# Optimization experiments

Measured on AMD Instinct MI355X. Metric: run time of the kernel, lower is better.

## Reference

```python
import jax, jax.numpy as jnp
import numpy as np

B, T, D_MODEL, D_HIDDEN, MAX_SEQLEN = 4, 2048, 1024, 256, 2048


def setup_inputs() -> dict:
    key = jax.random.key(0)
    ks = jax.random.split(key, 8)
    s_in = 1.0 / np.sqrt(D_MODEL)
    s_out = 1.0 / np.sqrt(D_HIDDEN)
    # xavier_uniform bound for W_bias (fan_in = fan_out = MAX_SEQLEN)
    xb = np.sqrt(6.0 / (MAX_SEQLEN + MAX_SEQLEN))
    return {
        "q": jax.random.normal(ks[0], (B, T, D_MODEL), jnp.float32),
        "k": jax.random.normal(ks[1], (B, T, D_MODEL), jnp.float32),
        "v": jax.random.normal(ks[2], (B, T, D_MODEL), jnp.float32),
        "Wq": jax.random.normal(ks[3], (D_MODEL, D_HIDDEN), jnp.float32) * s_in,
        "Wk": jax.random.normal(ks[4], (D_MODEL, D_HIDDEN), jnp.float32) * s_in,
        "Wv": jax.random.normal(ks[5], (D_MODEL, D_HIDDEN), jnp.float32) * s_in,
        "Wo": jax.random.normal(ks[6], (D_HIDDEN, D_MODEL), jnp.float32) * s_out,
        "W_bias": jax.random.uniform(ks[7], (MAX_SEQLEN, MAX_SEQLEN), jnp.float32, -xb, xb),
    }


def reference(q, k, v, Wq, Wk, Wv, Wo, W_bias):
    Ti, Tj = q.shape[1], k.shape[1]
    Q = q @ Wq                      # [B,Ti,dh]
    K = k @ Wk                      # [B,Tj,dh]
    V = v @ Wv                      # [B,Tj,dh]
    pos_bias = W_bias[:Ti, :Tj][None]               # [1,Ti,Tj]
    # NOTE: source subtracts max over dim 0 (batch). For pos_bias that dim is 1,
    # so exp_pos_bias == exp(0) == ones -- reproduced faithfully here.
    max_key = jnp.max(K, axis=0, keepdims=True)      # [1,Tj,dh]
    max_pos_bias = jnp.max(pos_bias, axis=0, keepdims=True)
    exp_key = jnp.exp(K - max_key)                   # [B,Tj,dh]
    exp_pos_bias = jnp.exp(pos_bias - max_pos_bias)  # [1,Ti,Tj]
    num = jnp.einsum('ij,bjd->bid', exp_pos_bias[0], exp_key * V)  # [B,Ti,dh]
    den = jnp.einsum('ij,bjd->bid', exp_pos_bias[0], exp_key)      # [B,Ti,dh]
    Yt = jax.nn.sigmoid(Q) * num / den
    return Yt @ Wo                  # [B,Ti,d_model]
```

## Files before the change

kernel.cpp:

```cpp
#include <hip/hip_runtime.h>
#include <hip/hip_bf16.h>
#include <math.h>

#define B_   4
#define T_   2048
#define DM   1024
#define DH   256
#define M_   (B_*T_)

typedef __bf16 bf16;
typedef __attribute__((ext_vector_type(8))) __bf16 bf16x8;
typedef __attribute__((ext_vector_type(4))) float  f32x4;

__device__ inline float sigmoidf_(float x) { return 1.0f / (1.0f + __expf(-x)); }

__device__ inline int swz8(int r, int c) { return (((c >> 3) ^ (r & 7)) << 3); }

__global__ void transpose_cvt_all(const float* __restrict__ Wq, const float* __restrict__ Wk,
                                  const float* __restrict__ Wv, const float* __restrict__ Wo,
                                  bf16* __restrict__ Wq_t, bf16* __restrict__ Wk_t,
                                  bf16* __restrict__ Wv_t, bf16* __restrict__ Wo_t,
                                  float* __restrict__ nd)
{
    const int bid = blockIdx.x;
    if (bid >= 1024) {
        nd[(bid - 1024) * 256 + threadIdx.x] = 0.f;
        return;
    }
    __shared__ float tile[32][33];
    const int w = bid >> 8, t = bid & 255;
    const float* in; bf16* out; int R, C, sh;
    if      (w == 0) { in = Wq; out = Wq_t; R = DM; C = DH; sh = 3; }
    else if (w == 1) { in = Wk; out = Wk_t; R = DM; C = DH; sh = 3; }
    else if (w == 2) { in = Wv; out = Wv_t; R = DM; C = DH; sh = 3; }
    else             { in = Wo; out = Wo_t; R = DH; C = DM; sh = 5; }
    const int r0 = (t >> sh) * 32, c0 = (t & ((1 << sh) - 1)) * 32;
    const int tx = threadIdx.x & 31, ty = threadIdx.x >> 5;
    #pragma unroll
    for (int i = ty; i < 32; i += 8)
        tile[i][tx] = in[(long)(r0 + i) * C + c0 + tx];
    __syncthreads();
    #pragma unroll
    for (int i = ty; i < 32; i += 8)
        out[(long)(c0 + i) * R + r0 + tx] = (bf16)tile[tx][i];
}

__global__ __launch_bounds__(512, 6)
void gemm_proj(const float* __restrict__ qin, const float* __restrict__ kin,
               const float* __restrict__ vin,
               const bf16* __restrict__ Wq_t, const bf16* __restrict__ Wk_t,
               const bf16* __restrict__ Wv_t,
               bf16* __restrict__ Yb, bf16* __restrict__ Kb, bf16* __restrict__ Vb)
{
    __shared__ __align__(16) bf16 As[2][64][64];
    __shared__ __align__(16) bf16 Bs[2][128][64];

    const int z = blockIdx.z;
    const float* A  = (z == 0) ? qin  : (z == 1) ? kin  : vin;
    const bf16*  Wt = (z == 0) ? Wq_t : (z == 1) ? Wk_t : Wv_t;
    bf16*        C  = (z == 0) ? Yb   : (z == 1) ? Kb   : Vb;

    const int bid  = blockIdx.x;
    const int tile = (bid & 7) * 32 + (bid >> 3);
    const int m0 = (tile >> 1) * 64;
    const int n0 = (tile & 1) * 128;

    const int tid = threadIdx.x, lane = tid & 63, wave = tid >> 6;
    const int wr = wave >> 2, wc = wave & 3;
    const int q4 = lane >> 4, l16 = lane & 15;

    f32x4 acc[2][2] = {};
    const int ar = tid >> 3, ac8 = (tid & 7) * 8;
    const int br = tid >> 2, bc16 = (tid & 3) * 16;

    const float* aBase = &A[(long)(m0 + ar) * DM + ac8];
    const bf16*  bBase = &Wt[(long)(n0 + br) * DM + bc16];

    f32x4  pa0[2], pa1[2];
    bf16x8 pb0[2], pb1[2];
    #pragma unroll
    for (int p = 0; p < 2; ++p) {
        const float* ap = aBase + p * 64;
        pa0[p] = *(const f32x4*)ap; pa1[p] = *(const f32x4*)(ap + 4);
        const bf16* bp = bBase + p * 64;
        pb0[p] = *(const bf16x8*)bp; pb1[p] = *(const bf16x8*)(bp + 8);
    }
    {
        bf16x8 o;
        #pragma unroll
        for (int e = 0; e < 4; ++e) { o[e] = (bf16)pa0[0][e]; o[4 + e] = (bf16)pa1[0][e]; }
        *(bf16x8*)&As[0][ar][swz8(ar, ac8)]      = o;
        *(bf16x8*)&Bs[0][br][swz8(br, bc16)]     = pb0[0];
        *(bf16x8*)&Bs[0][br][swz8(br, bc16 + 8)] = pb1[0];
    }
    __syncthreads();

    #pragma unroll
    for (int s = 0; s < 16; ++s) {
        const int cs = s & 1;
        const int ns = cs ^ 1;
        if (s + 2 < 16) {
            const float* ap = aBase + (s + 2) * 64;
            pa0[cs] = *(const f32x4*)ap; pa1[cs] = *(const f32x4*)(ap + 4);
            const bf16* bp = bBase + (s + 2) * 64;
            pb0[cs] = *(const bf16x8*)bp; pb1[cs] = *(const bf16x8*)(bp + 8);
        }
        if (s + 1 < 16) {
            bf16x8 o;
            #pragma unroll
            for (int e = 0; e < 4; ++e) { o[e] = (bf16)pa0[ns][e]; o[4 + e] = (bf16)pa1[ns][e]; }
            *(bf16x8*)&As[ns][ar][swz8(ar, ac8)]      = o;
            *(bf16x8*)&Bs[ns][br][swz8(br, bc16)]     = pb0[ns];
            *(bf16x8*)&Bs[ns][br][swz8(br, bc16 + 8)] = pb1[ns];
        }
        #pragma unroll
        for (int kk = 0; kk < 64; kk += 32) {
            const int ra = wr * 32 + l16, rb = wc * 32 + l16;
            bf16x8 a0 = *(const bf16x8*)&As[cs][ra     ][swz8(ra,      kk + q4 * 8)];
            bf16x8 a1 = *(const bf16x8*)&As[cs][ra + 16][swz8(ra + 16, kk + q4 * 8)];
            bf16x8 b0 = *(const bf16x8*)&Bs[cs][rb     ][swz8(rb,      kk + q4 * 8)];
            bf16x8 b1 = *(const bf16x8*)&Bs[cs][rb + 16][swz8(rb + 16, kk + q4 * 8)];
            acc[0][0] = __builtin_amdgcn_mfma_f32_16x16x32_bf16(a0, b0, acc[0][0], 0, 0, 0);
            acc[0][1] = __builtin_amdgcn_mfma_f32_16x16x32_bf16(a0, b1, acc[0][1], 0, 0, 0);
            acc[1][0] = __builtin_amdgcn_mfma_f32_16x16x32_bf16(a1, b0, acc[1][0], 0, 0, 0);
            acc[1][1] = __builtin_amdgcn_mfma_f32_16x16x32_bf16(a1, b1, acc[1][1], 0, 0, 0);
        }
        __syncthreads();
    }
    #pragma unroll
    for (int i = 0; i < 2; ++i)
        #pragma unroll
        for (int j = 0; j < 2; ++j)
            #pragma unroll
            for (int r = 0; r < 4; ++r) {
                int gm = m0 + wr * 32 + i * 16 + q4 * 4 + r;
                int gn = n0 + wc * 32 + j * 16 + l16;
                float v = acc[i][j][r];
                C[(long)gm * DH + gn] = (bf16)((z == 0) ? sigmoidf_(v) : v);
            }
}

__global__ void reduce_kv(const bf16* __restrict__ Kb, const bf16* __restrict__ Vb,
                          float* __restrict__ numb, float* __restrict__ denb)
{
    __shared__ float red[2][4][B_][DH];
    const int tid = threadIdx.x;
    const int g = tid & 31, jj = tid >> 5;
    const int d8 = g * 8;
    const int j = blockIdx.x * 8 + jj;

    bf16x8 kx[B_], vx[B_];
    #pragma unroll
    for (int b = 0; b < B_; ++b) {
        kx[b] = *(const bf16x8*)&Kb[((long)b * T_ + j) * DH + d8];
        vx[b] = *(const bf16x8*)&Vb[((long)b * T_ + j) * DH + d8];
    }
    float sn[B_][8], sd[B_][8];
    #pragma unroll
    for (int e = 0; e < 8; ++e) {
        float k0 = (float)kx[0][e], k1 = (float)kx[1][e];
        float k2 = (float)kx[2][e], k3 = (float)kx[3][e];
        float mx = fmaxf(fmaxf(k0, k1), fmaxf(k2, k3));
        float e0 = __expf(k0 - mx), e1 = __expf(k1 - mx);
        float e2 = __expf(k2 - mx), e3 = __expf(k3 - mx);
        sn[0][e] = e0 * (float)vx[0][e]; sd[0][e] = e0;
        sn[1][e] = e1 * (float)vx[1][e]; sd[1][e] = e1;
        sn[2][e] = e2 * (float)vx[2][e]; sd[2][e] = e2;
        sn[3][e] = e3 * (float)vx[3][e]; sd[3][e] = e3;
    }
    #pragma unroll
    for (int b = 0; b < B_; ++b)
        #pragma unroll
        for (int e = 0; e < 8; ++e) {
            sn[b][e] += __shfl_xor(sn[b][e], 32);
            sd[b][e] += __shfl_xor(sd[b][e], 32);
        }
    const int w = tid >> 6;
    if ((tid & 32) == 0) {
        #pragma unroll
        for (int b = 0; b < B_; ++b)
            #pragma unroll
            for (int e = 0; e < 8; ++e) {
                red[0][w][b][d8 + e] = sn[b][e];
                red[1][w][b][d8 + e] = sd[b][e];
            }
    }
    __syncthreads();
    #pragma unroll
    for (int o = tid; o < 2 * B_ * DH; o += 256) {
        const int arr = o >> 10, b = (o >> 8) & 3, d = o & 255;
        float s = red[arr][0][b][d] + red[arr][1][b][d]
                + red[arr][2][b][d] + red[arr][3][b][d];
        float* dst = (o < 1024) ? &numb[o] : &denb[o - 1024];
        atomicAdd(dst, s);
    }
}

__global__ __launch_bounds__(512, 6)
void gemm_out(const bf16* __restrict__ Yb, const bf16* __restrict__ Wo_t,
              const float* __restrict__ numb, const float* __restrict__ denb,
              float* __restrict__ out)
{
    __shared__ __align__(16) bf16 As[2][64][64];
    __shared__ __align__(16) bf16 Bs[2][128][64];
    __shared__ float rv_s[DH];

    const int bid  = blockIdx.x;
    const int tile = (bid & 7) * 128 + (bid >> 3);
    const int m0 = (tile >> 3) * 64;
    const int n0 = (tile & 7) * 128;
    const int b  = m0 >> 11;

    const int tid = threadIdx.x, lane = tid & 63, wave = tid >> 6;
    const int wr = wave >> 2, wc = wave & 3;
    const int q4 = lane >> 4, l16 = lane & 15;

    if (tid < DH) rv_s[tid] = numb[b * DH + tid] / denb[b * DH + tid];

    f32x4 acc[2][2] = {};
    const int ar = tid >> 3, ac8 = (tid & 7) * 8;
    const int br = tid >> 2, bc16 = (tid & 3) * 16;

    const bf16* aBase = &Yb[(long)(m0 + ar) * DH + ac8];
    const bf16* bBase = &Wo_t[(long)(n0 + br) * DH + bc16];

    bf16x8 pq[2], pb0[2], pb1[2];
    #pragma unroll
    for (int p = 0; p < 2; ++p) {
        pq[p]  = *(const bf16x8*)(aBase + p * 64);
        const bf16* wp = bBase + p * 64;
        pb0[p] = *(const bf16x8*)wp; pb1[p] = *(const bf16x8*)(wp + 8);
    }
    __syncthreads();
    {
        bf16x8 o;
        #pragma unroll
        for (int e = 0; e < 8; ++e)
            o[e] = (bf16)((float)pq[0][e] * rv_s[ac8 + e]);
        *(bf16x8*)&As[0][ar][swz8(ar, ac8)]      = o;
        *(bf16x8*)&Bs[0][br][swz8(br, bc16)]     = pb0[0];
        *(bf16x8*)&Bs[0][br][swz8(br, bc16 + 8)] = pb1[0];
    }
    __syncthreads();

    #pragma unroll
    for (int s = 0; s < 4; ++s) {
        const int cs = s & 1, ns = cs ^ 1;
        if (s + 2 < 4) {
            pq[cs]  = *(const bf16x8*)(aBase + (s + 2) * 64);
            const bf16* wp = bBase + (s + 2) * 64;
            pb0[cs] = *(const bf16x8*)wp; pb1[cs] = *(const bf16x8*)(wp + 8);
        }
        if (s + 1 < 4) {
            bf16x8 o;
            #pragma unroll
            for (int e = 0; e < 8; ++e)
                o[e] = (bf16)((float)pq[ns][e] * rv_s[(s + 1) * 64 + ac8 + e]);
            *(bf16x8*)&As[ns][ar][swz8(ar, ac8)]      = o;
            *(bf16x8*)&Bs[ns][br][swz8(br, bc16)]     = pb0[ns];
            *(bf16x8*)&Bs[ns][br][swz8(br, bc16 + 8)] = pb1[ns];
        }
        #pragma unroll
        for (int kk = 0; kk < 64; kk += 32) {
            const int ra = wr * 32 + l16, rb = wc * 32 + l16;
            bf16x8 a0 = *(const bf16x8*)&As[cs][ra     ][swz8(ra,      kk + q4 * 8)];
            bf16x8 a1 = *(const bf16x8*)&As[cs][ra + 16][swz8(ra + 16, kk + q4 * 8)];
            bf16x8 b0 = *(const bf16x8*)&Bs[cs][rb     ][swz8(rb,      kk + q4 * 8)];
            bf16x8 b1 = *(const bf16x8*)&Bs[cs][rb + 16][swz8(rb + 16, kk + q4 * 8)];
            acc[0][0] = __builtin_amdgcn_mfma_f32_16x16x32_bf16(a0, b0, acc[0][0], 0, 0, 0);
            acc[0][1] = __builtin_amdgcn_mfma_f32_16x16x32_bf16(a0, b1, acc[0][1], 0, 0, 0);
            acc[1][0] = __builtin_amdgcn_mfma_f32_16x16x32_bf16(a1, b0, acc[1][0], 0, 0, 0);
            acc[1][1] = __builtin_amdgcn_mfma_f32_16x16x32_bf16(a1, b1, acc[1][1], 0, 0, 0);
        }
        __syncthreads();
    }
    #pragma unroll
    for (int i = 0; i < 2; ++i)
        #pragma unroll
        for (int j = 0; j < 2; ++j)
            #pragma unroll
            for (int r = 0; r < 4; ++r) {
                int gm = m0 + wr * 32 + i * 16 + q4 * 4 + r;
                int gn = n0 + wc * 32 + j * 16 + l16;
                out[(long)gm * DM + gn] = acc[i][j][r];
            }
}

extern "C" void kernel_launch(void* const* d_in, const int* in_sizes, int n_in,
                              void* d_out, int out_size, void* d_ws, size_t ws_size,
                              hipStream_t stream)
{
    const float* q  = (const float*)d_in[0];
    const float* k  = (const float*)d_in[1];
    const float* v  = (const float*)d_in[2];
    const float* Wq = (const float*)d_in[3];
    const float* Wk = (const float*)d_in[4];
    const float* Wv = (const float*)d_in[5];
    const float* Wo = (const float*)d_in[6];
    float* out = (float*)d_out;

    char* ws = (char*)d_ws;
    bf16* Yb    = (bf16*)ws;  ws += (size_t)M_ * DH * sizeof(bf16);
    bf16* Kb    = (bf16*)ws;  ws += (size_t)M_ * DH * sizeof(bf16);
    bf16* Vb    = (bf16*)ws;  ws += (size_t)M_ * DH * sizeof(bf16);
    bf16* Wq_t  = (bf16*)ws;  ws += (size_t)DM * DH * sizeof(bf16);
    bf16* Wk_t  = (bf16*)ws;  ws += (size_t)DM * DH * sizeof(bf16);
    bf16* Wv_t  = (bf16*)ws;  ws += (size_t)DM * DH * sizeof(bf16);
    bf16* Wo_t  = (bf16*)ws;  ws += (size_t)DM * DH * sizeof(bf16);
    float* numb = (float*)ws; ws += (size_t)B_ * DH * sizeof(float);
    float* denb = (float*)ws; ws += (size_t)B_ * DH * sizeof(float);

    transpose_cvt_all<<<1032, 256, 0, stream>>>(Wq, Wk, Wv, Wo,
                                                Wq_t, Wk_t, Wv_t, Wo_t, numb);

    gemm_proj<<<dim3(256, 1, 3), 512, 0, stream>>>(q, k, v, Wq_t, Wk_t, Wv_t,
                                                   Yb, Kb, Vb);
    reduce_kv<<<256, 256, 0, stream>>>(Kb, Vb, numb, denb);
    gemm_out<<<1024, 512, 0, stream>>>(Yb, Wo_t, numb, denb, out);
}
```

Baseline: 193.3 us.

## Use direct global-to-LDS loads and fold num/den scale into per-batch Wo

Weight tiles in both GEMMs are now loaded with global_load_lds direct-to-LDS transfers using pre-swizzled source addresses, instead of going through registers. The num/den ratio is no longer applied to Y tiles inside gemm_out. A new scale_wo kernel multiplies it into a per-batch bf16 copy of Wo stored in the dead Kb buffer. gemm_out then stages its output through LDS to issue coalesced 16-byte stores. This removes register staging and per-element scaling from the inner loop, at the cost of an extra kernel launch, an extra Wo copy per batch, and a projection loop rewritten with manual unrolling.

```diff
diff --git a/kernel.cpp b/kernel.cpp
--- a/kernel.cpp
+++ b/kernel.cpp
@@ -15,6 +15,12 @@
 __device__ inline float sigmoidf_(float x) { return 1.0f / (1.0f + __expf(-x)); }
 
 __device__ inline int swz8(int r, int c) { return (((c >> 3) ^ (r & 7)) << 3); }
+
+__device__ inline void gload16(const void* g, void* l) {
+    __builtin_amdgcn_global_load_lds(
+        (const __attribute__((address_space(1))) void*)g,
+        (__attribute__((address_space(3))) void*)l, 16, 0, 0);
+}
 
 __global__ void transpose_cvt_all(const float* __restrict__ Wq, const float* __restrict__ Wk,
                                   const float* __restrict__ Wv, const float* __restrict__ Wo,
@@ -68,50 +74,213 @@
     const int tid = threadIdx.x, lane = tid & 63, wave = tid >> 6;
     const int wr = wave >> 2, wc = wave & 3;
     const int q4 = lane >> 4, l16 = lane & 15;
+    const int lr = lane >> 3, lc = lane & 7;
 
     f32x4 acc[2][2] = {};
     const int ar = tid >> 3, ac8 = (tid & 7) * 8;
-    const int br = tid >> 2, bc16 = (tid & 3) * 16;
 
     const float* aBase = &A[(long)(m0 + ar) * DM + ac8];
-    const bf16*  bBase = &Wt[(long)(n0 + br) * DM + bc16];
-
-    f32x4  pa0[2], pa1[2];
-    bf16x8 pb0[2], pb1[2];
-    #pragma unroll
-    for (int p = 0; p < 2; ++p) {
-        const float* ap = aBase + p * 64;
-        pa0[p] = *(const f32x4*)ap; pa1[p] = *(const f32x4*)(ap + 4);
-        const bf16* bp = bBase + p * 64;
-        pb0[p] = *(const bf16x8*)bp; pb1[p] = *(const bf16x8*)(bp + 8);
-    }
+
+    const int br0 = wave * 8 + lr, br1 = 64 + wave * 8 + lr;
+    const bf16* bSrc0 = &Wt[(long)(n0 + br0) * DM + ((lc ^ (br0 & 7)) * 8)];
+    const bf16* bSrc1 = &Wt[(long)(n0 + br1) * DM + ((lc ^ (br1 & 7)) * 8)];
+
+    f32x4 a0A = *(const f32x4*)(aBase);
+    f32x4 a1A = *(const f32x4*)(aBase + 4);
+    f32x4 a0B = *(const f32x4*)(aBase + 64);
+    f32x4 a1B = *(const f32x4*)(aBase + 68);
+
     {
+        gload16(bSrc0, &Bs[0][wave * 8][0]);
+        gload16(bSrc1, &Bs[0][64 + wave * 8][0]);
         bf16x8 o;
         #pragma unroll
-        for (int e = 0; e < 4; ++e) { o[e] = (bf16)pa0[0][e]; o[4 + e] = (bf16)pa1[0][e]; }
-        *(bf16x8*)&As[0][ar][swz8(ar, ac8)]      = o;
-        *(bf16x8*)&Bs[0][br][swz8(br, bc16)]     = pb0[0];
-        *(bf16x8*)&Bs[0][br][swz8(br, bc16 + 8)] = pb1[0];
-    }
-    __syncthreads();
-
-    #pragma unroll
-    for (int s = 0; s < 16; ++s) {
-        const int cs = s & 1;
-        const int ns = cs ^ 1;
-        if (s + 2 < 16) {
-            const float* ap = aBase + (s + 2) * 64;
-            pa0[cs] = *(const f32x4*)ap; pa1[cs] = *(const f32x4*)(ap + 4);
-            const bf16* bp = bBase + (s + 2) * 64;
-            pb0[cs] = *(const bf16x8*)bp; pb1[cs] = *(const bf16x8*)(bp + 8);
-        }
-        if (s + 1 < 16) {
+        for (int e = 0; e < 4; ++e) { o[e] = (bf16)a0A[e]; o[4 + e] = (bf16)a1A[e]; }
+        *(bf16x8*)&As[0][ar][swz8(ar, ac8)] = o;
+    }
+    __syncthreads();
+
+    #define MFMA_SLAB(BUF)                                                              \
+        _Pragma("unroll")                                                               \
+        for (int kk = 0; kk < 64; kk += 32) {                                           \
+            const int ra = wr * 32 + l16, rb = wc * 32 + l16;                           \
+            bf16x8 a0 = *(const bf16x8*)&As[BUF][ra     ][swz8(ra,      kk + q4 * 8)];  \
+            bf16x8 a1 = *(const bf16x8*)&As[BUF][ra + 16][swz8(ra + 16, kk + q4 * 8)];  \
+            bf16x8 b0 = *(const bf16x8*)&Bs[BUF][rb     ][swz8(rb,      kk + q4 * 8)];  \
+            bf16x8 b1 = *(const bf16x8*)&Bs[BUF][rb + 16][swz8(rb + 16, kk + q4 * 8)];  \
+            acc[0][0] = __builtin_amdgcn_mfma_f32_16x16x32_bf16(a0, b0, acc[0][0], 0, 0, 0); \
+            acc[0][1] = __builtin_amdgcn_mfma_f32_16x16x32_bf16(a0, b1, acc[0][1], 0, 0, 0); \
+            acc[1][0] = __builtin_amdgcn_mfma_f32_16x16x32_bf16(a1, b0, acc[1][0], 0, 0, 0); \
+            acc[1][1] = __builtin_amdgcn_mfma_f32_16x16x32_bf16(a1, b1, acc[1][1], 0, 0, 0); \
+        }
+
+    for (int p = 0; p < 8; ++p) {
+        const int e = 2 * p;
+        {
+            gload16(bSrc0 + (e + 1) * 64, &Bs[1][wave * 8][0]);
+            gload16(bSrc1 + (e + 1) * 64, &Bs[1][64 + wave * 8][0]);
             bf16x8 o;
             #pragma unroll
-            for (int e = 0; e < 4; ++e) { o[e] = (bf16)pa0[ns][e]; o[4 + e] = (bf16)pa1[ns][e]; }
-            *(bf16x8*)&As[ns][ar][swz8(ar, ac8)]      = o;
-            *(bf16x8*)&Bs[ns][br][swz8(br, bc16)]     = pb0[ns];
-            *(bf16x8*)&Bs[ns][br][swz8(br, bc16 + 8)] = pb1[ns];
+            for (int ee = 0; ee < 4; ++ee) { o[ee] = (bf16)a0B[ee]; o[4 + ee] = (bf16)a1B[ee]; }
+            *(bf16x8*)&As[1][ar][swz8(ar, ac8)] = o;
+            if (e + 2 < 16) {
+                a0A = *(const f32x4*)(aBase + (e + 2) * 64);
+                a1A = *(const f32x4*)(aBase + (e + 2) * 64 + 4);
+            }
+            MFMA_SLAB(0)
+            __syncthreads();
+        }
+        const int o_ = e + 1;
+        {
+            if (o_ + 1 < 16) {
+                gload16(bSrc0 + (o_ + 1) * 64, &Bs[0][wave * 8][0]);
+                gload16(bSrc1 + (o_ + 1) * 64, &Bs[0][64 + wave * 8][0]);
+                bf16x8 o;
+                #pragma unroll
+                for (int ee = 0; ee < 4; ++ee) { o[ee] = (bf16)a0A[ee]; o[4 + ee] = (bf16)a1A[ee]; }
+                *(bf16x8*)&As[0][ar][swz8(ar, ac8)] = o;
+            }
+            if (o_ + 2 < 16) {
+                a0B = *(const f32x4*)(aBase + (o_ + 2) * 64);
+                a1B = *(const f32x4*)(aBase + (o_ + 2) * 64 + 4);
+            }
+            MFMA_SLAB(1)
+            if (o_ < 15) __syncthreads();
+        }
+    }
+    #undef MFMA_SLAB
+
+    #pragma unroll
+    for (int i = 0; i < 2; ++i)
+        #pragma unroll
+        for (int j = 0; j < 2; ++j)
+            #pragma unroll
+            for (int r = 0; r < 4; ++r) {
+                int gm = m0 + wr * 32 + i * 16 + q4 * 4 + r;
+                int gn = n0 + wc * 32 + j * 16 + l16;
+                float v = acc[i][j][r];
+                C[(long)gm * DH + gn] = (bf16)((z == 0) ? sigmoidf_(v) : v);
+            }
+}
+
+__global__ void reduce_kv(const bf16* __restrict__ Kb, const bf16* __restrict__ Vb,
+                          float* __restrict__ numb, float* __restrict__ denb)
+{
+    __shared__ float red[2][4][B_][DH];
+    const int tid = threadIdx.x;
+    const int g = tid & 31, jj = tid >> 5;
+    const int d8 = g * 8;
+    const int j = blockIdx.x * 8 + jj;
+
+    bf16x8 kx[B_], vx[B_];
+    #pragma unroll
+    for (int b = 0; b < B_; ++b) {
+        kx[b] = *(const bf16x8*)&Kb[((long)b * T_ + j) * DH + d8];
+        vx[b] = *(const bf16x8*)&Vb[((long)b * T_ + j) * DH + d8];
+    }
+    float sn[B_][8], sd[B_][8];
+    #pragma unroll
+    for (int e = 0; e < 8; ++e) {
+        float k0 = (float)kx[0][e], k1 = (float)kx[1][e];
+        float k2 = (float)kx[2][e], k3 = (float)kx[3][e];
+        float mx = fmaxf(fmaxf(k0, k1), fmaxf(k2, k3));
+        float e0 = __expf(k0 - mx), e1 = __expf(k1 - mx);
+        float e2 = __expf(k2 - mx), e3 = __expf(k3 - mx);
+        sn[0][e] = e0 * (float)vx[0][e]; sd[0][e] = e0;
+        sn[1][e] = e1 * (float)vx[1][e]; sd[1][e] = e1;
+        sn[2][e] = e2 * (float)vx[2][e]; sd[2][e] = e2;
+        sn[3][e] = e3 * (float)vx[3][e]; sd[3][e] = e3;
+    }
+    #pragma unroll
+    for (int b = 0; b < B_; ++b)
+        #pragma unroll
+        for (int e = 0; e < 8; ++e) {
+            sn[b][e] += __shfl_xor(sn[b][e], 32);
+            sd[b][e] += __shfl_xor(sd[b][e], 32);
+        }
+    const int w = tid >> 6;
+    if ((tid & 32) == 0) {
+        #pragma unroll
+        for (int b = 0; b < B_; ++b)
+            #pragma unroll
+            for (int e = 0; e < 8; ++e) {
+                red[0][w][b][d8 + e] = sn[b][e];
+                red[1][w][b][d8 + e] = sd[b][e];
+            }
+    }
+    __syncthreads();
+    #pragma unroll
+    for (int o = tid; o < 2 * B_ * DH; o += 256) {
+        const int arr = o >> 10, b = (o >> 8) & 3, d = o & 255;
+        float s = red[arr][0][b][d] + red[arr][1][b][d]
+                + red[arr][2][b][d] + red[arr][3][b][d];
+        float* dst = (o < 1024) ? &numb[o] : &denb[o - 1024];
+        atomicAdd(dst, s);
+    }
+}
+
+__global__ void scale_wo(const bf16* __restrict__ Wo_t, const float* __restrict__ numb,
+                         const float* __restrict__ denb, bf16* __restrict__ Wo_b)
+{
+    const int t = blockIdx.x * 256 + threadIdx.x;
+    const int n = t >> 5, d8 = (t & 31) * 8;
+    bf16x8 w = *(const bf16x8*)&Wo_t[((long)n << 8) + d8];
+    #pragma unroll
+    for (int b = 0; b < B_; ++b) {
+        f32x4 nv0 = *(const f32x4*)&numb[b * DH + d8];
+        f32x4 nv1 = *(const f32x4*)&numb[b * DH + d8 + 4];
+        f32x4 dv0 = *(const f32x4*)&denb[b * DH + d8];
+        f32x4 dv1 = *(const f32x4*)&denb[b * DH + d8 + 4];
+        bf16x8 o;
+        #pragma unroll
+        for (int e = 0; e < 4; ++e) {
+            o[e]     = (bf16)((float)w[e]     * (nv0[e] / dv0[e]));
+            o[4 + e] = (bf16)((float)w[4 + e] * (nv1[e] / dv1[e]));
+        }
+        *(bf16x8*)&Wo_b[((long)b << 18) + ((long)n << 8) + d8] = o;
+    }
+}
+
+__global__ __launch_bounds__(512, 6)
+void gemm_out(const bf16* __restrict__ Yb, const bf16* __restrict__ Wo_b,
+              float* __restrict__ out)
+{
+    __shared__ __align__(16) char smem[49152];
+    auto As = reinterpret_cast<bf16 (*)[64][64]>(smem);
+    auto Bs = reinterpret_cast<bf16 (*)[128][64]>(smem + 16384);
+    auto Cb = reinterpret_cast<float (*)[132]>(smem);
+
+    const int bid  = blockIdx.x;
+    const int tile = (bid & 7) * 128 + (bid >> 3);
+    const int m0 = (tile >> 3) * 64;
+    const int n0 = (tile & 7) * 128;
+    const int b  = m0 >> 11;
+
+    const int tid = threadIdx.x, lane = tid & 63, wave = tid >> 6;
+    const int wr = wave >> 2, wc = wave & 3;
+    const int q4 = lane >> 4, l16 = lane & 15;
+    const int lr = lane >> 3, lc = lane & 7;
+
+    f32x4 acc[2][2] = {};
+
+    const int arw = wave * 8 + lr;
+    const int br0 = wave * 8 + lr, br1 = 64 + wave * 8 + lr;
+    const bf16* aSrc  = &Yb[((long)(m0 + arw) << 8) + ((lc ^ (arw & 7)) * 8)];
+    const bf16* bSrc0 = &Wo_b[((long)b << 18) + ((long)(n0 + br0) << 8) + ((lc ^ (br0 & 7)) * 8)];
+    const bf16* bSrc1 = &Wo_b[((long)b << 18) + ((long)(n0 + br1) << 8) + ((lc ^ (br1 & 7)) * 8)];
+
+    gload16(aSrc,  &As[0][wave * 8][0]);
+    gload16(bSrc0, &Bs[0][wave * 8][0]);
+    gload16(bSrc1, &Bs[0][64 + wave * 8][0]);
+    __syncthreads();
+
+    #pragma unroll
+    for (int s = 0; s < 4; ++s) {
+        const int cs = s & 1, ns = cs ^ 1;
+        if (s + 1 < 4) {
+            gload16(aSrc  + (s + 1) * 64, &As[ns][wave * 8][0]);
+            gload16(bSrc0 + (s + 1) * 64, &Bs[ns][wave * 8][0]);
+            gload16(bSrc1 + (s + 1) * 64, &Bs[ns][64 + wave * 8][0]);
         }
         #pragma unroll
         for (int kk = 0; kk < 64; kk += 32) {
@@ -127,163 +296,20 @@
         }
         __syncthreads();
     }
+
     #pragma unroll
     for (int i = 0; i < 2; ++i)
         #pragma unroll
         for (int j = 0; j < 2; ++j)
             #pragma unroll
-            for (int r = 0; r < 4; ++r) {
-                int gm = m0 + wr * 32 + i * 16 + q4 * 4 + r;
-                int gn = n0 + wc * 32 + j * 16 + l16;
-                float v = acc[i][j][r];
-                C[(long)gm * DH + gn] = (bf16)((z == 0) ? sigmoidf_(v) : v);
-            }
-}
-
-__global__ void reduce_kv(const bf16* __restrict__ Kb, const bf16* __restrict__ Vb,
-                          float* __restrict__ numb, float* __restrict__ denb)
-{
-    __shared__ float red[2][4][B_][DH];
-    const int tid = threadIdx.x;
-    const int g = tid & 31, jj = tid >> 5;
-    const int d8 = g * 8;
-    const int j = blockIdx.x * 8 + jj;
-
-    bf16x8 kx[B_], vx[B_];
-    #pragma unroll
-    for (int b = 0; b < B_; ++b) {
-        kx[b] = *(const bf16x8*)&Kb[((long)b * T_ + j) * DH + d8];
-        vx[b] = *(const bf16x8*)&Vb[((long)b * T_ + j) * DH + d8];
-    }
-    float sn[B_][8], sd[B_][8];
-    #pragma unroll
-    for (int e = 0; e < 8; ++e) {
-        float k0 = (float)kx[0][e], k1 = (float)kx[1][e];
-        float k2 = (float)kx[2][e], k3 = (float)kx[3][e];
-        float mx = fmaxf(fmaxf(k0, k1), fmaxf(k2, k3));
-        float e0 = __expf(k0 - mx), e1 = __expf(k1 - mx);
-        float e2 = __expf(k2 - mx), e3 = __expf(k3 - mx);
-        sn[0][e] = e0 * (float)vx[0][e]; sd[0][e] = e0;
-        sn[1][e] = e1 * (float)vx[1][e]; sd[1][e] = e1;
-        sn[2][e] = e2 * (float)vx[2][e]; sd[2][e] = e2;
-        sn[3][e] = e3 * (float)vx[3][e]; sd[3][e] = e3;
-    }
-    #pragma unroll
-    for (int b = 0; b < B_; ++b)
-        #pragma unroll
-        for (int e = 0; e < 8; ++e) {
-            sn[b][e] += __shfl_xor(sn[b][e], 32);
-            sd[b][e] += __shfl_xor(sd[b][e], 32);
-        }
-    const int w = tid >> 6;
-    if ((tid & 32) == 0) {
-        #pragma unroll
-        for (int b = 0; b < B_; ++b)
-            #pragma unroll
-            for (int e = 0; e < 8; ++e) {
-                red[0][w][b][d8 + e] = sn[b][e];
-                red[1][w][b][d8 + e] = sd[b][e];
-            }
-    }
-    __syncthreads();
-    #pragma unroll
-    for (int o = tid; o < 2 * B_ * DH; o += 256) {
-        const int arr = o >> 10, b = (o >> 8) & 3, d = o & 255;
-        float s = red[arr][0][b][d] + red[arr][1][b][d]
-                + red[arr][2][b][d] + red[arr][3][b][d];
-        float* dst = (o < 1024) ? &numb[o] : &denb[o - 1024];
-        atomicAdd(dst, s);
-    }
-}
-
-__global__ __launch_bounds__(512, 6)
-void gemm_out(const bf16* __restrict__ Yb, const bf16* __restrict__ Wo_t,
-              const float* __restrict__ numb, const float* __restrict__ denb,
-              float* __restrict__ out)
-{
-    __shared__ __align__(16) bf16 As[2][64][64];
-    __shared__ __align__(16) bf16 Bs[2][128][64];
-    __shared__ float rv_s[DH];
-
-    const int bid  = blockIdx.x;
-    const int tile = (bid & 7) * 128 + (bid >> 3);
-    const int m0 = (tile >> 3) * 64;
-    const int n0 = (tile & 7) * 128;
-    const int b  = m0 >> 11;
-
-    const int tid = threadIdx.x, lane = tid & 63, wave = tid >> 6;
-    const int wr = wave >> 2, wc = wave & 3;
-    const int q4 = lane >> 4, l16 = lane & 15;
-
-    if (tid < DH) rv_s[tid] = numb[b * DH + tid] / denb[b * DH + tid];
-
-    f32x4 acc[2][2] = {};
-    const int ar = tid >> 3, ac8 = (tid & 7) * 8;
-    const int br = tid >> 2, bc16 = (tid & 3) * 16;
-
-    const bf16* aBase = &Yb[(long)(m0 + ar) * DH + ac8];
-    const bf16* bBase = &Wo_t[(long)(n0 + br) * DH + bc16];
-
-    bf16x8 pq[2], pb0[2], pb1[2];
-    #pragma unroll
-    for (int p = 0; p < 2; ++p) {
-        pq[p]  = *(const bf16x8*)(aBase + p * 64);
-        const bf16* wp = bBase + p * 64;
-        pb0[p] = *(const bf16x8*)wp; pb1[p] = *(const bf16x8*)(wp + 8);
-    }
-    __syncthreads();
-    {
-        bf16x8 o;
-        #pragma unroll
-        for (int e = 0; e < 8; ++e)
-            o[e] = (bf16)((float)pq[0][e] * rv_s[ac8 + e]);
-        *(bf16x8*)&As[0][ar][swz8(ar, ac8)]      = o;
-        *(bf16x8*)&Bs[0][br][swz8(br, bc16)]     = pb0[0];
-        *(bf16x8*)&Bs[0][br][swz8(br, bc16 + 8)] = pb1[0];
-    }
-    __syncthreads();
-
-    #pragma unroll
-    for (int s = 0; s < 4; ++s) {
-        const int cs = s & 1, ns = cs ^ 1;
-        if (s + 2 < 4) {
-            pq[cs]  = *(const bf16x8*)(aBase + (s + 2) * 64);
-            const bf16* wp = bBase + (s + 2) * 64;
-            pb0[cs] = *(const bf16x8*)wp; pb1[cs] = *(const bf16x8*)(wp + 8);
-        }
-        if (s + 1 < 4) {
-            bf16x8 o;
-            #pragma unroll
-            for (int e = 0; e < 8; ++e)
-                o[e] = (bf16)((float)pq[ns][e] * rv_s[(s + 1) * 64 + ac8 + e]);
-            *(bf16x8*)&As[ns][ar][swz8(ar, ac8)]      = o;
-            *(bf16x8*)&Bs[ns][br][swz8(br, bc16)]     = pb0[ns];
-            *(bf16x8*)&Bs[ns][br][swz8(br, bc16 + 8)] = pb1[ns];
-        }
-        #pragma unroll
-        for (int kk = 0; kk < 64; kk += 32) {
-            const int ra = wr * 32 + l16, rb = wc * 32 + l16;
-            bf16x8 a0 = *(const bf16x8*)&As[cs][ra     ][swz8(ra,      kk + q4 * 8)];
-            bf16x8 a1 = *(const bf16x8*)&As[cs][ra + 16][swz8(ra + 16, kk + q4 * 8)];
-            bf16x8 b0 = *(const bf16x8*)&Bs[cs][rb     ][swz8(rb,      kk + q4 * 8)];
-            bf16x8 b1 = *(const bf16x8*)&Bs[cs][rb + 16][swz8(rb + 16, kk + q4 * 8)];
-            acc[0][0] = __builtin_amdgcn_mfma_f32_16x16x32_bf16(a0, b0, acc[0][0], 0, 0, 0);
-            acc[0][1] = __builtin_amdgcn_mfma_f32_16x16x32_bf16(a0, b1, acc[0][1], 0, 0, 0);
-            acc[1][0] = __builtin_amdgcn_mfma_f32_16x16x32_bf16(a1, b0, acc[1][0], 0, 0, 0);
-            acc[1][1] = __builtin_amdgcn_mfma_f32_16x16x32_bf16(a1, b1, acc[1][1], 0, 0, 0);
-        }
-        __syncthreads();
-    }
-    #pragma unroll
-    for (int i = 0; i < 2; ++i)
-        #pragma unroll
-        for (int j = 0; j < 2; ++j)
-            #pragma unroll
-            for (int r = 0; r < 4; ++r) {
-                int gm = m0 + wr * 32 + i * 16 + q4 * 4 + r;
-                int gn = n0 + wc * 32 + j * 16 + l16;
-                out[(long)gm * DM + gn] = acc[i][j][r];
-            }
+            for (int r = 0; r < 4; ++r)
+                Cb[wr * 32 + i * 16 + q4 * 4 + r][wc * 32 + j * 16 + l16] = acc[i][j][r];
+    __syncthreads();
+    const int orow = tid >> 3, oc = (tid & 7) * 4;
+    float* orp = &out[(long)(m0 + orow) * DM + n0];
+    #pragma unroll
+    for (int c2 = 0; c2 < 4; ++c2)
+        *(f32x4*)&orp[oc + 32 * c2] = *(const f32x4*)&Cb[orow][oc + 32 * c2];
 }
 
 extern "C" void kernel_launch(void* const* d_in, const int* in_sizes, int n_in,
@@ -309,6 +335,7 @@
     bf16* Wo_t  = (bf16*)ws;  ws += (size_t)DM * DH * sizeof(bf16);
     float* numb = (float*)ws; ws += (size_t)B_ * DH * sizeof(float);
     float* denb = (float*)ws; ws += (size_t)B_ * DH * sizeof(float);
+    bf16* Wo_b  = Kb;
 
     transpose_cvt_all<<<1032, 256, 0, stream>>>(Wq, Wk, Wv, Wo,
                                                 Wq_t, Wk_t, Wv_t, Wo_t, numb);
@@ -316,5 +343,6 @@
     gemm_proj<<<dim3(256, 1, 3), 512, 0, stream>>>(q, k, v, Wq_t, Wk_t, Wv_t,
                                                    Yb, Kb, Vb);
     reduce_kv<<<256, 256, 0, stream>>>(Kb, Vb, numb, denb);
-    gemm_out<<<1024, 512, 0, stream>>>(Yb, Wo_t, numb, denb, out);
-}
+    scale_wo<<<128, 256, 0, stream>>>(Wo_t, numb, denb, Wo_b);
+    gemm_out<<<1024, 512, 0, stream>>>(Yb, Wo_b, out);
+}
```

Result: no change. 195.9 us (+1.4%).

## Enlarge GEMM tiles to 128x128, DMA weights to LDS, stage epilogue stores

Applied to the files above, without the earlier changes.

Both GEMMs move from 64x128 tiles with 8 waves to 128x128 tiles with 4 waves, each wave holding a 4x4 grid of MFMA accumulators. This raises data reuse per LDS load and cuts the number of blocks. Weight tiles are now loaded directly into LDS with global_load_lds, and outputs are staged through LDS so global stores are coalesced and vectorized. reduce_kv now has each block accumulate four row groups, which cuts its grid and atomic traffic. In exchange, the larger tiles leave fewer blocks (384 for proj, 512 for out), which may lower occupancy and load balance on the 256-CU part.

```diff
diff --git a/kernel.cpp b/kernel.cpp
--- a/kernel.cpp
+++ b/kernel.cpp
@@ -15,6 +15,12 @@
 __device__ inline float sigmoidf_(float x) { return 1.0f / (1.0f + __expf(-x)); }
 
 __device__ inline int swz8(int r, int c) { return (((c >> 3) ^ (r & 7)) << 3); }
+
+__device__ inline void gload16(const void* g, void* l) {
+    __builtin_amdgcn_global_load_lds(
+        (const __attribute__((address_space(1))) void*)g,
+        (__attribute__((address_space(3))) void*)l, 16, 0, 0);
+}
 
 __global__ void transpose_cvt_all(const float* __restrict__ Wq, const float* __restrict__ Wk,
                                   const float* __restrict__ Wv, const float* __restrict__ Wo,
@@ -45,15 +51,16 @@
         out[(long)(c0 + i) * R + r0 + tx] = (bf16)tile[tx][i];
 }
 
-__global__ __launch_bounds__(512, 6)
+__global__ __launch_bounds__(256, 2)
 void gemm_proj(const float* __restrict__ qin, const float* __restrict__ kin,
                const float* __restrict__ vin,
                const bf16* __restrict__ Wq_t, const bf16* __restrict__ Wk_t,
                const bf16* __restrict__ Wv_t,
                bf16* __restrict__ Yb, bf16* __restrict__ Kb, bf16* __restrict__ Vb)
 {
-    __shared__ __align__(16) bf16 As[2][64][64];
-    __shared__ __align__(16) bf16 Bs[2][128][64];
+    __shared__ __align__(16) char smem[65536];
+    auto As = reinterpret_cast<bf16 (*)[128][64]>(smem);
+    auto Bs = reinterpret_cast<bf16 (*)[128][64]>(smem + 32768);
 
     const int z = blockIdx.z;
     const float* A  = (z == 0) ? qin  : (z == 1) ? kin  : vin;
@@ -61,83 +68,90 @@
     bf16*        C  = (z == 0) ? Yb   : (z == 1) ? Kb   : Vb;
 
     const int bid  = blockIdx.x;
-    const int tile = (bid & 7) * 32 + (bid >> 3);
-    const int m0 = (tile >> 1) * 64;
+    const int tile = (bid & 7) * 16 + (bid >> 3);
+    const int m0 = (tile >> 1) * 128;
     const int n0 = (tile & 1) * 128;
 
     const int tid = threadIdx.x, lane = tid & 63, wave = tid >> 6;
-    const int wr = wave >> 2, wc = wave & 3;
+    const int wr = wave >> 1, wc = wave & 1;
     const int q4 = lane >> 4, l16 = lane & 15;
 
-    f32x4 acc[2][2] = {};
-    const int ar = tid >> 3, ac8 = (tid & 7) * 8;
-    const int br = tid >> 2, bc16 = (tid & 3) * 16;
-
-    const float* aBase = &A[(long)(m0 + ar) * DM + ac8];
-    const bf16*  bBase = &Wt[(long)(n0 + br) * DM + bc16];
-
-    f32x4  pa0[2], pa1[2];
-    bf16x8 pb0[2], pb1[2];
-    #pragma unroll
-    for (int p = 0; p < 2; ++p) {
-        const float* ap = aBase + p * 64;
-        pa0[p] = *(const f32x4*)ap; pa1[p] = *(const f32x4*)(ap + 4);
-        const bf16* bp = bBase + p * 64;
-        pb0[p] = *(const bf16x8*)bp; pb1[p] = *(const bf16x8*)(bp + 8);
-    }
-    {
-        bf16x8 o;
-        #pragma unroll
-        for (int e = 0; e < 4; ++e) { o[e] = (bf16)pa0[0][e]; o[4 + e] = (bf16)pa1[0][e]; }
-        *(bf16x8*)&As[0][ar][swz8(ar, ac8)]      = o;
-        *(bf16x8*)&Bs[0][br][swz8(br, bc16)]     = pb0[0];
-        *(bf16x8*)&Bs[0][br][swz8(br, bc16 + 8)] = pb1[0];
-    }
-    __syncthreads();
-
-    #pragma unroll
-    for (int s = 0; s < 16; ++s) {
-        const int cs = s & 1;
-        const int ns = cs ^ 1;
-        if (s + 2 < 16) {
-            const float* ap = aBase + (s + 2) * 64;
-            pa0[cs] = *(const f32x4*)ap; pa1[cs] = *(const f32x4*)(ap + 4);
-            const bf16* bp = bBase + (s + 2) * 64;
-            pb0[cs] = *(const bf16x8*)bp; pb1[cs] = *(const bf16x8*)(bp + 8);
-        }
-        if (s + 1 < 16) {
-            bf16x8 o;
-            #pragma unroll
-            for (int e = 0; e < 4; ++e) { o[e] = (bf16)pa0[ns][e]; o[4 + e] = (bf16)pa1[ns][e]; }
-            *(bf16x8*)&As[ns][ar][swz8(ar, ac8)]      = o;
-            *(bf16x8*)&Bs[ns][br][swz8(br, bc16)]     = pb0[ns];
-            *(bf16x8*)&Bs[ns][br][swz8(br, bc16 + 8)] = pb1[ns];
-        }
-        #pragma unroll
-        for (int kk = 0; kk < 64; kk += 32) {
-            const int ra = wr * 32 + l16, rb = wc * 32 + l16;
-            bf16x8 a0 = *(const bf16x8*)&As[cs][ra     ][swz8(ra,      kk + q4 * 8)];
-            bf16x8 a1 = *(const bf16x8*)&As[cs][ra + 16][swz8(ra + 16, kk + q4 * 8)];
-            bf16x8 b0 = *(const bf16x8*)&Bs[cs][rb     ][swz8(rb,      kk + q4 * 8)];
-            bf16x8 b1 = *(const bf16x8*)&Bs[cs][rb + 16][swz8(rb + 16, kk + q4 * 8)];
-            acc[0][0] = __builtin_amdgcn_mfma_f32_16x16x32_bf16(a0, b0, acc[0][0], 0, 0, 0);
-            acc[0][1] = __builtin_amdgcn_mfma_f32_16x16x32_bf16(a0, b1, acc[0][1], 0, 0, 0);
-            acc[1][0] = __builtin_amdgcn_mfma_f32_16x16x32_bf16(a1, b0, acc[1][0], 0, 0, 0);
-            acc[1][1] = __builtin_amdgcn_mfma_f32_16x16x32_bf16(a1, b1, acc[1][1], 0, 0, 0);
-        }
+    f32x4 acc[4][4] = {};
+
+    const int arow = tid >> 1, acb = (tid & 1) * 32;
+    const float* aBase = &A[(long)(m0 + arow) * DM + acb];
+
+    const bf16* bS[4];
+    #pragma unroll
+    for (int i = 0; i < 4; ++i) {
+        const int brow = wave * 32 + i * 8 + (lane >> 3);
+        bS[i] = &Wt[(long)(n0 + brow) * DM + (((lane & 7) ^ (brow & 7)) * 8)];
+    }
+
+    f32x4 rA[8], rB[8];
+
+    #define LOAD_A(slot, s) { _Pragma("unroll") for (int c = 0; c < 8; ++c) \
+        slot[c] = *(const f32x4*)(aBase + (s) * 64 + c * 4); }
+    #define STAGE_A(slot, buf) { _Pragma("unroll") for (int c = 0; c < 4; ++c) { \
+        bf16x8 o_; _Pragma("unroll") for (int e = 0; e < 4; ++e) { \
+            o_[e] = (bf16)slot[2*c][e]; o_[4+e] = (bf16)slot[2*c+1][e]; } \
+        *(bf16x8*)&As[buf][arow][swz8(arow, acb + c * 8)] = o_; } }
+    #define DMA_B(buf, s) { _Pragma("unroll") for (int i = 0; i < 4; ++i) \
+        gload16(bS[i] + (s) * 64, &Bs[buf][wave * 32 + i * 8][0]); }
+    #define MFMA_SLAB(buf) { _Pragma("unroll") for (int kk = 0; kk < 64; kk += 32) { \
+        bf16x8 af[4], bfr[4]; \
+        _Pragma("unroll") for (int mi = 0; mi < 4; ++mi) { \
+            const int ra = wr * 64 + mi * 16 + l16; \
+            af[mi] = *(const bf16x8*)&As[buf][ra][swz8(ra, kk + q4 * 8)]; } \
+        _Pragma("unroll") for (int ni = 0; ni < 4; ++ni) { \
+            const int rb = wc * 64 + ni * 16 + l16; \
+            bfr[ni] = *(const bf16x8*)&Bs[buf][rb][swz8(rb, kk + q4 * 8)]; } \
+        _Pragma("unroll") for (int mi = 0; mi < 4; ++mi) \
+            _Pragma("unroll") for (int ni = 0; ni < 4; ++ni) \
+                acc[mi][ni] = __builtin_amdgcn_mfma_f32_16x16x32_bf16(af[mi], bfr[ni], acc[mi][ni], 0, 0, 0); } }
+
+    LOAD_A(rA, 0);
+    DMA_B(0, 0);
+    STAGE_A(rA, 0);
+    LOAD_A(rB, 1);
+    __syncthreads();
+
+    for (int p = 0; p < 8; ++p) {
+        const int e = 2 * p;
+        DMA_B(1, e + 1);
+        STAGE_A(rB, 1);
+        if (e + 2 < 16) LOAD_A(rA, e + 2);
+        MFMA_SLAB(0);
         __syncthreads();
-    }
-    #pragma unroll
-    for (int i = 0; i < 2; ++i)
-        #pragma unroll
-        for (int j = 0; j < 2; ++j)
+        if (e + 2 < 16) { DMA_B(0, e + 2); STAGE_A(rA, 0); }
+        if (e + 3 < 16) LOAD_A(rB, e + 3);
+        MFMA_SLAB(1);
+        if (p < 7) __syncthreads();
+    }
+    #undef LOAD_A
+    #undef STAGE_A
+    #undef DMA_B
+
+    __syncthreads();
+    auto Cb = reinterpret_cast<bf16 (*)[136]>(smem);
+    #pragma unroll
+    for (int mi = 0; mi < 4; ++mi)
+        #pragma unroll
+        for (int ni = 0; ni < 4; ++ni)
             #pragma unroll
             for (int r = 0; r < 4; ++r) {
-                int gm = m0 + wr * 32 + i * 16 + q4 * 4 + r;
-                int gn = n0 + wc * 32 + j * 16 + l16;
-                float v = acc[i][j][r];
-                C[(long)gm * DH + gn] = (bf16)((z == 0) ? sigmoidf_(v) : v);
+                float v = acc[mi][ni][r];
+                if (z == 0) v = sigmoidf_(v);
+                Cb[wr * 64 + mi * 16 + q4 * 4 + r][wc * 64 + ni * 16 + l16] = (bf16)v;
             }
+    __syncthreads();
+    {
+        const int row = tid >> 1, cb = (tid & 1) * 64;
+        bf16* dst = &C[(long)(m0 + row) * DH + n0 + cb];
+        #pragma unroll
+        for (int c = 0; c < 8; ++c)
+            *(bf16x8*)&dst[c * 8] = *(const bf16x8*)&Cb[row][cb + c * 8];
+    }
 }
 
 __global__ void reduce_kv(const bf16* __restrict__ Kb, const bf16* __restrict__ Vb,
@@ -147,26 +161,28 @@
     const int tid = threadIdx.x;
     const int g = tid & 31, jj = tid >> 5;
     const int d8 = g * 8;
-    const int j = blockIdx.x * 8 + jj;
-
-    bf16x8 kx[B_], vx[B_];
-    #pragma unroll
-    for (int b = 0; b < B_; ++b) {
-        kx[b] = *(const bf16x8*)&Kb[((long)b * T_ + j) * DH + d8];
-        vx[b] = *(const bf16x8*)&Vb[((long)b * T_ + j) * DH + d8];
-    }
-    float sn[B_][8], sd[B_][8];
-    #pragma unroll
-    for (int e = 0; e < 8; ++e) {
-        float k0 = (float)kx[0][e], k1 = (float)kx[1][e];
-        float k2 = (float)kx[2][e], k3 = (float)kx[3][e];
-        float mx = fmaxf(fmaxf(k0, k1), fmaxf(k2, k3));
-        float e0 = __expf(k0 - mx), e1 = __expf(k1 - mx);
-        float e2 = __expf(k2 - mx), e3 = __expf(k3 - mx);
-        sn[0][e] = e0 * (float)vx[0][e]; sd[0][e] = e0;
-        sn[1][e] = e1 * (float)vx[1][e]; sd[1][e] = e1;
-        sn[2][e] = e2 * (float)vx[2][e]; sd[2][e] = e2;
-        sn[3][e] = e3 * (float)vx[3][e]; sd[3][e] = e3;
+
+    float sn[B_][8] = {}, sd[B_][8] = {};
+    for (int t4 = 0; t4 < 4; ++t4) {
+        const int j = blockIdx.x * 32 + t4 * 8 + jj;
+        bf16x8 kx[B_], vx[B_];
+        #pragma unroll
+        for (int b = 0; b < B_; ++b) {
+            kx[b] = *(const bf16x8*)&Kb[((long)b * T_ + j) * DH + d8];
+            vx[b] = *(const bf16x8*)&Vb[((long)b * T_ + j) * DH + d8];
+        }
+        #pragma unroll
+        for (int e = 0; e < 8; ++e) {
+            float k0 = (float)kx[0][e], k1 = (float)kx[1][e];
+            float k2 = (float)kx[2][e], k3 = (float)kx[3][e];
+            float mx = fmaxf(fmaxf(k0, k1), fmaxf(k2, k3));
+            float e0 = __expf(k0 - mx), e1 = __expf(k1 - mx);
+            float e2 = __expf(k2 - mx), e3 = __expf(k3 - mx);
+            sn[0][e] += e0 * (float)vx[0][e]; sd[0][e] += e0;
+            sn[1][e] += e1 * (float)vx[1][e]; sd[1][e] += e1;
+            sn[2][e] += e2 * (float)vx[2][e]; sd[2][e] += e2;
+            sn[3][e] += e3 * (float)vx[3][e]; sd[3][e] += e3;
+        }
     }
     #pragma unroll
     for (int b = 0; b < B_; ++b)
@@ -196,94 +212,106 @@
     }
 }
 
-__global__ __launch_bounds__(512, 6)
+__global__ __launch_bounds__(256, 2)
 void gemm_out(const bf16* __restrict__ Yb, const bf16* __restrict__ Wo_t,
               const float* __restrict__ numb, const float* __restrict__ denb,
               float* __restrict__ out)
 {
-    __shared__ __align__(16) bf16 As[2][64][64];
-    __shared__ __align__(16) bf16 Bs[2][128][64];
+    __shared__ __align__(16) char smem[65536];
+    auto As = reinterpret_cast<bf16 (*)[128][64]>(smem);
+    auto Bs = reinterpret_cast<bf16 (*)[128][64]>(smem + 32768);
     __shared__ float rv_s[DH];
 
     const int bid  = blockIdx.x;
-    const int tile = (bid & 7) * 128 + (bid >> 3);
-    const int m0 = (tile >> 3) * 64;
+    const int tile = (bid & 7) * 64 + (bid >> 3);
+    const int m0 = (tile >> 3) * 128;
     const int n0 = (tile & 7) * 128;
     const int b  = m0 >> 11;
 
     const int tid = threadIdx.x, lane = tid & 63, wave = tid >> 6;
-    const int wr = wave >> 2, wc = wave & 3;
+    const int wr = wave >> 1, wc = wave & 1;
     const int q4 = lane >> 4, l16 = lane & 15;
 
-    if (tid < DH) rv_s[tid] = numb[b * DH + tid] / denb[b * DH + tid];
-
-    f32x4 acc[2][2] = {};
-    const int ar = tid >> 3, ac8 = (tid & 7) * 8;
-    const int br = tid >> 2, bc16 = (tid & 3) * 16;
-
-    const bf16* aBase = &Yb[(long)(m0 + ar) * DH + ac8];
-    const bf16* bBase = &Wo_t[(long)(n0 + br) * DH + bc16];
-
-    bf16x8 pq[2], pb0[2], pb1[2];
-    #pragma unroll
-    for (int p = 0; p < 2; ++p) {
-        pq[p]  = *(const bf16x8*)(aBase + p * 64);
-        const bf16* wp = bBase + p * 64;
-        pb0[p] = *(const bf16x8*)wp; pb1[p] = *(const bf16x8*)(wp + 8);
-    }
-    __syncthreads();
-    {
-        bf16x8 o;
-        #pragma unroll
-        for (int e = 0; e < 8; ++e)
-            o[e] = (bf16)((float)pq[0][e] * rv_s[ac8 + e]);
-        *(bf16x8*)&As[0][ar][swz8(ar, ac8)]      = o;
-        *(bf16x8*)&Bs[0][br][swz8(br, bc16)]     = pb0[0];
-        *(bf16x8*)&Bs[0][br][swz8(br, bc16 + 8)] = pb1[0];
-    }
-    __syncthreads();
-
-    #pragma unroll
-    for (int s = 0; s < 4; ++s) {
-        const int cs = s & 1, ns = cs ^ 1;
-        if (s + 2 < 4) {
-            pq[cs]  = *(const bf16x8*)(aBase + (s + 2) * 64);
-            const bf16* wp = bBase + (s + 2) * 64;
-            pb0[cs] = *(const bf16x8*)wp; pb1[cs] = *(const bf16x8*)(wp + 8);
-        }
-        if (s + 1 < 4) {
-            bf16x8 o;
+    rv_s[tid] = numb[b * DH + tid] / denb[b * DH + tid];
+
+    f32x4 acc[4][4] = {};
+
+    const int arow = tid >> 1, acb = (tid & 1) * 32;
+    const bf16* aBase = &Yb[(long)(m0 + arow) * DH + acb];
+
+    const bf16* bS[4];
+    #pragma unroll
+    for (int i = 0; i < 4; ++i) {
+        const int brow = wave * 32 + i * 8 + (lane >> 3);
+        bS[i] = &Wo_t[(long)(n0 + brow) * DH + (((lane & 7) ^ (brow & 7)) * 8)];
+    }
+
+    bf16x8 rQA[4], rQB[4];
+    #define LOAD_Q(slot, s) { _Pragma("unroll") for (int c = 0; c < 4; ++c) \
+        slot[c] = *(const bf16x8*)(aBase + (s) * 64 + c * 8); }
+    #define STAGE_Q(slot, buf, s) { _Pragma("unroll") for (int c = 0; c < 4; ++c) { \
+        bf16x8 o_; _Pragma("unroll") for (int e = 0; e < 8; ++e) \
+            o_[e] = (bf16)((float)slot[c][e] * rv_s[(s) * 64 + acb + c * 8 + e]); \
+        *(bf16x8*)&As[buf][arow][swz8(arow, acb + c * 8)] = o_; } }
+    #define DMA_B(buf, s) { _Pragma("unroll") for (int i = 0; i < 4; ++i) \
+        gload16(bS[i] + (s) * 64, &Bs[buf][wave * 32 + i * 8][0]); }
+    #define MFMA_SLAB(buf) { _Pragma("unroll") for (int kk = 0; kk < 64; kk += 32) { \
+        bf16x8 af[4], bfr[4]; \
+        _Pragma("unroll") for (int mi = 0; mi < 4; ++mi) { \
+            const int ra = wr * 64 + mi * 16 + l16; \
+            af[mi] = *(const bf16x8*)&As[buf][ra][swz8(ra, kk + q4 * 8)]; } \
+        _Pragma("unroll") for (int ni = 0; ni < 4; ++ni) { \
+            const int rb = wc * 64 + ni * 16 + l16; \
+            bfr[ni] = *(const bf16x8*)&Bs[buf][rb][swz8(rb, kk + q4 * 8)]; } \
+        _Pragma("unroll") for (int mi = 0; mi < 4; ++mi) \
+            _Pragma("unroll") for (int ni = 0; ni < 4; ++ni) \
+                acc[mi][ni] = __builtin_amdgcn_mfma_f32_16x16x32_bf16(af[mi], bfr[ni], acc[mi][ni], 0, 0, 0); } }
+
+    LOAD_Q(rQA, 0);
+    LOAD_Q(rQB, 1);
+    DMA_B(0, 0);
+    __syncthreads();
+    STAGE_Q(rQA, 0, 0);
+    DMA_B(1, 1);
+    LOAD_Q(rQA, 2);
+    __syncthreads();
+    STAGE_Q(rQB, 1, 1);
+    LOAD_Q(rQB, 3);
+    MFMA_SLAB(0);
+    __syncthreads();
+    DMA_B(0, 2);
+    STAGE_Q(rQA, 0, 2);
+    MFMA_SLAB(1);
+    __syncthreads();
+    DMA_B(1, 3);
+    STAGE_Q(rQB, 1, 3);
+    MFMA_SLAB(0);
+    __syncthreads();
+    MFMA_SLAB(1);
+    #undef LOAD_Q
+    #undef STAGE_Q
+    #undef DMA_B
+
+    auto Cbf = reinterpret_cast<float (*)[132]>(smem);
+    #pragma unroll
+    for (int h = 0; h < 2; ++h) {
+        __syncthreads();
+        if (wr == h) {
             #pragma unroll
-            for (int e = 0; e < 8; ++e)
-                o[e] = (bf16)((float)pq[ns][e] * rv_s[(s + 1) * 64 + ac8 + e]);
-            *(bf16x8*)&As[ns][ar][swz8(ar, ac8)]      = o;
-            *(bf16x8*)&Bs[ns][br][swz8(br, bc16)]     = pb0[ns];
-            *(bf16x8*)&Bs[ns][br][swz8(br, bc16 + 8)] = pb1[ns];
-        }
-        #pragma unroll
-        for (int kk = 0; kk < 64; kk += 32) {
-            const int ra = wr * 32 + l16, rb = wc * 32 + l16;
-            bf16x8 a0 = *(const bf16x8*)&As[cs][ra     ][swz8(ra,      kk + q4 * 8)];
-            bf16x8 a1 = *(const bf16x8*)&As[cs][ra + 16][swz8(ra + 16, kk + q4 * 8)];
-            bf16x8 b0 = *(const bf16x8*)&Bs[cs][rb     ][swz8(rb,      kk + q4 * 8)];
-            bf16x8 b1 = *(const bf16x8*)&Bs[cs][rb + 16][swz8(rb + 16, kk + q4 * 8)];
-            acc[0][0] = __builtin_amdgcn_mfma_f32_16x16x32_bf16(a0, b0, acc[0][0], 0, 0, 0);
-            acc[0][1] = __builtin_amdgcn_mfma_f32_16x16x32_bf16(a0, b1, acc[0][1], 0, 0, 0);
-            acc[1][0] = __builtin_amdgcn_mfma_f32_16x16x32_bf16(a1, b0, acc[1][0], 0, 0, 0);
-            acc[1][1] = __builtin_amdgcn_mfma_f32_16x16x32_bf16(a1, b1, acc[1][1], 0, 0, 0);
+            for (int mi = 0; mi < 4; ++mi)
+                #pragma unroll
+                for (int ni = 0; ni < 4; ++ni)
+                    #pragma unroll
+                    for (int r = 0; r < 4; ++r)
+                        Cbf[mi * 16 + q4 * 4 + r][wc * 64 + ni * 16 + l16] = acc[mi][ni][r];
         }
         __syncthreads();
-    }
-    #pragma unroll
-    for (int i = 0; i < 2; ++i)
-        #pragma unroll
-        for (int j = 0; j < 2; ++j)
-            #pragma unroll
-            for (int r = 0; r < 4; ++r) {
-                int gm = m0 + wr * 32 + i * 16 + q4 * 4 + r;
-                int gn = n0 + wc * 32 + j * 16 + l16;
-                out[(long)gm * DM + gn] = acc[i][j][r];
-            }
+        const int row = tid >> 2, cb = (tid & 3) * 32;
+        float* dst = &out[(long)(m0 + h * 64 + row) * DM + n0 + cb];
+        #pragma unroll
+        for (int c = 0; c < 8; ++c)
+            *(f32x4*)&dst[c * 4] = *(const f32x4*)&Cbf[row][cb + c * 4];
+    }
 }
 
 extern "C" void kernel_launch(void* const* d_in, const int* in_sizes, int n_in,
@@ -313,8 +341,8 @@
     transpose_cvt_all<<<1032, 256, 0, stream>>>(Wq, Wk, Wv, Wo,
                                                 Wq_t, Wk_t, Wv_t, Wo_t, numb);
 
-    gemm_proj<<<dim3(256, 1, 3), 512, 0, stream>>>(q, k, v, Wq_t, Wk_t, Wv_t,
+    gemm_proj<<<dim3(128, 1, 3), 256, 0, stream>>>(q, k, v, Wq_t, Wk_t, Wv_t,
                                                    Yb, Kb, Vb);
-    reduce_kv<<<256, 256, 0, stream>>>(Kb, Vb, numb, denb);
-    gemm_out<<<1024, 512, 0, stream>>>(Yb, Wo_t, numb, denb, out);
-}
+    reduce_kv<<<64, 256, 0, stream>>>(Kb, Vb, numb, denb);
+    gemm_out<<<512, 256, 0, stream>>>(Yb, Wo_t, numb, denb, out);
+}
```

After: 221.4 us. 14.6% more time.
